# Kernel optimization log

Hardware: AMD Instinct MI355X
Metric: run time of the kernel (lower is better)

Reference implementation:

```python
import jax, jax.numpy as jnp
import numpy as np

B, S, D, H, F = 2, 2048, 1024, 16, 4096
HD = D // H
NEG_INF = jnp.float32(-1e30)


def layer_norm(x, gamma, beta, eps=1e-6):
    mu = jnp.mean(x, axis=-1, keepdims=True)
    var = jnp.mean(jnp.square(x - mu), axis=-1, keepdims=True)
    return (x - mu) * jax.lax.rsqrt(var + eps) * gamma + beta


def setup_inputs() -> dict:
    key = jax.random.key(0)
    ks = jax.random.split(key, 8)
    d = np.sqrt(float(D))
    dx_up = np.sqrt(6.0 / (D + F))
    dx_dn = np.sqrt(6.0 / (F + D))
    return {
        "x_embeds": jax.random.normal(ks[0], (B, S, D), dtype=jnp.float32),
        "tokens": jax.random.randint(ks[1], (B, S), 0, 128, dtype=jnp.int32),
        "KQV": jax.random.uniform(ks[2], (D, 3 * D), jnp.float32, -1 / d, 1 / d),
        "WO": jax.random.uniform(ks[3], (D, D), jnp.float32, -1 / d, 1 / d),
        "W_up": jax.random.uniform(ks[4], (D, F), jnp.float32, -dx_up, dx_up),
        "b_up": jnp.zeros((F,), jnp.float32),
        "W_down": jax.random.uniform(ks[5], (F, D), jnp.float32, -dx_dn, dx_dn),
        "b_down": jnp.zeros((D,), jnp.float32),
        "ln1_g": jnp.ones((D,), jnp.float32),
        "ln1_b": jnp.zeros((D,), jnp.float32),
        "ln2_g": jnp.ones((D,), jnp.float32),
        "ln2_b": jnp.zeros((D,), jnp.float32),
        "start_token_id": 1,
    }


def reference(x_embeds, tokens, KQV, WO, W_up, b_up, W_down, b_down,
              ln1_g, ln1_b, ln2_g, ln2_b, start_token_id):
    b, s = x_embeds.shape[0], x_embeds.shape[1]
    # --- attention ---
    x_kqv = jnp.einsum("bsd,de->bse", x_embeds, KQV)          # [B,S,3D]
    x_kqv = x_kqv.reshape(b, s, H, 3, HD)
    k = x_kqv[:, :, :, 0, :]   # [B,S,H,HD]
    q = x_kqv[:, :, :, 1, :]
    v = x_kqv[:, :, :, 2, :]
    inner = jnp.einsum("bqhd,bkhd->bhqk", q, k)               # [B,H,S,S]
    # causal mask
    causal = jnp.tril(jnp.ones((s, s), dtype=bool))           # [S,S]
    # block-diagonal document mask from start tokens
    seg = jnp.cumsum((tokens == start_token_id).astype(jnp.int32), axis=1)  # [B,S]
    same_seg = seg[:, :, None] == seg[:, None, :]             # [B,S,S]
    mask = causal[None, None] & same_seg[:, None]             # [B,1->H,S,S]
    inner = jnp.where(mask, inner, NEG_INF)
    dk = jnp.sqrt(jnp.float32(HD))
    WA = jax.nn.softmax(inner / dk, axis=-1)
    head_outs = jnp.einsum("bhqk,bkhd->bqhd", WA, v)          # [B,S,H,HD]
    out = head_outs.reshape(b, s, D) @ WO
    out = layer_norm(out, ln1_g, ln1_b)
    x = out + x_embeds
    # --- ffnn ---
    h = jax.nn.relu(x @ W_up + b_up)
    out = h @ W_down + b_down
    out = layer_norm(out, ln2_g, ln2_b)
    return out + x
```

## Files before the change

### kernel.cpp

```cpp
#include <hip/hip_runtime.h>

typedef unsigned short u16;
typedef unsigned int u32;
typedef __bf16 bf16_t;
typedef bf16_t bf16x8 __attribute__((ext_vector_type(8)));
typedef u16 u16x8 __attribute__((ext_vector_type(8)));
typedef float f32x4 __attribute__((ext_vector_type(4)));

__device__ __forceinline__ float bf2f(u16 u) {
    union { float f; unsigned i; } c; c.i = ((unsigned)u) << 16; return c.f;
}
__device__ __forceinline__ u16 f2bf(float f) {
    return __builtin_bit_cast(u16, (bf16_t)f);
}
__device__ __forceinline__ f32x4 mfma16(bf16x8 a, bf16x8 b, f32x4 c) {
    return __builtin_amdgcn_mfma_f32_16x16x32_bf16(a, b, c, 0, 0, 0);
}
__device__ __forceinline__ void gld16(const u16* g, u16* l) {
    __builtin_amdgcn_global_load_lds(
        (const __attribute__((address_space(1))) void*)g,
        (__attribute__((address_space(3))) void*)l, 16, 0, 0);
}

__global__ __launch_bounds__(256)
void cvt_kernel(const float* __restrict__ in, u16* __restrict__ out)
{
    const int i = (blockIdx.x * 256 + threadIdx.x) * 8;
    float4 a = *reinterpret_cast<const float4*>(in + i);
    float4 b = *reinterpret_cast<const float4*>(in + i + 4);
    u16x8 o;
    o[0] = f2bf(a.x); o[1] = f2bf(a.y); o[2] = f2bf(a.z); o[3] = f2bf(a.w);
    o[4] = f2bf(b.x); o[5] = f2bf(b.y); o[6] = f2bf(b.z); o[7] = f2bf(b.w);
    *reinterpret_cast<u16x8*>(out + i) = o;
}

__global__ __launch_bounds__(256)
void cvt_t_kernel(const float* __restrict__ in, u16* __restrict__ out,
                  int K, int N)
{
    __shared__ float tile[32][33];
    const int kb = blockIdx.x * 32, nb = blockIdx.y * 32;
    const int r = threadIdx.x >> 3, c4 = threadIdx.x & 7;
    float4 v = *reinterpret_cast<const float4*>(&in[(size_t)(kb + r) * N + nb + c4 * 4]);
    tile[r][c4 * 4 + 0] = v.x; tile[r][c4 * 4 + 1] = v.y;
    tile[r][c4 * 4 + 2] = v.z; tile[r][c4 * 4 + 3] = v.w;
    __syncthreads();
    ushort4 o;
    o.x = f2bf(tile[c4 * 4 + 0][r]);
    o.y = f2bf(tile[c4 * 4 + 1][r]);
    o.z = f2bf(tile[c4 * 4 + 2][r]);
    o.w = f2bf(tile[c4 * 4 + 3][r]);
    *reinterpret_cast<ushort4*>(&out[(size_t)(nb + r) * K + kb + c4 * 4]) = o;
}

template<int NSPLIT, bool BIAS, bool RELU, bool QSCALE>
__global__ __launch_bounds__(512, 4)
void gemm8w_kernel(const u16* __restrict__ A, const u16* __restrict__ Bt,
                   const float* __restrict__ bias, u16* __restrict__ C,
                   int M, int N, int K)
{
    __shared__ u16 As[128][64];
    __shared__ u16 Bs[128][64];
    const int tid  = threadIdx.x;
    const int lane = tid & 63;
    const int wid  = tid >> 6;
    const int wm = wid >> 2, wn = wid & 3;
    const int bm = blockIdx.x, bn = blockIdx.y;
    const int kg = lane >> 4;
    const int lc = lane & 15;
    const int pk = kg ^ ((lc + (lc >> 2)) & 3);

    f32x4 acc[4][2];
    #pragma unroll
    for (int i = 0; i < 4; ++i)
        #pragma unroll
        for (int j = 0; j < 2; ++j)
            acc[i][j] = f32x4{0.f, 0.f, 0.f, 0.f};

    const int nk = (K >> 6) / NSPLIT;
    const int kbase = (NSPLIT > 1) ? blockIdx.z * nk : 0;

    for (int kt = 0; kt < nk; ++kt) {
        const int ktg = kbase + kt;
        __syncthreads();
        #pragma unroll
        for (int p = 0; p < 2; ++p) {
            int c = p * 512 + tid;
            int row  = c >> 3;
            int half = (c >> 2) & 1;
            int ko   = (((c & 3) ^ ((row + (row >> 2)) & 3)) << 3) + half * 32;
            gld16(A + (size_t)(bm * 128 + row) * K + ktg * 64 + ko,
                  &As[0][0] + c * 8);
            gld16(Bt + (size_t)(bn * 128 + row) * K + ktg * 64 + ko,
                  &Bs[0][0] + c * 8);
        }
        __syncthreads();

        bf16x8 af[4][2], bf[2][2];
        #pragma unroll
        for (int i = 0; i < 4; ++i)
            #pragma unroll
            for (int kk = 0; kk < 2; ++kk)
                af[i][kk] = *reinterpret_cast<const bf16x8*>(
                    &As[wm * 64 + i * 16 + lc][kk * 32 + pk * 8]);
        #pragma unroll
        for (int j = 0; j < 2; ++j)
            #pragma unroll
            for (int kk = 0; kk < 2; ++kk)
                bf[j][kk] = *reinterpret_cast<const bf16x8*>(
                    &Bs[wn * 32 + j * 16 + lc][kk * 32 + pk * 8]);
        #pragma unroll
        for (int j = 0; j < 2; ++j)
            #pragma unroll
            for (int i = 0; i < 4; ++i)
                #pragma unroll
                for (int kk = 0; kk < 2; ++kk)
                    acc[i][j] = mfma16(af[i][kk], bf[j][kk], acc[i][j]);
    }

    u16* Cp = C + (size_t)((NSPLIT > 1) ? blockIdx.z : 0) * M * N;
    const bool addb = BIAS && (NSPLIT == 1 || blockIdx.z == 0);
    #pragma unroll
    for (int i = 0; i < 4; ++i) {
        #pragma unroll
        for (int j = 0; j < 2; ++j) {
            int col = bn * 128 + wn * 32 + j * 16 + lc;
            float bv = addb ? bias[col] : 0.f;
            float qs = 1.0f;
            if (QSCALE) {
                u32 cm = (u32)col % 192u;
                if (cm >= 64u && cm < 128u) qs = 0.1803368875f;
            }
            #pragma unroll
            for (int r = 0; r < 4; ++r) {
                int row = bm * 128 + wm * 64 + i * 16 + kg * 4 + r;
                float v = acc[i][j][r] + bv;
                if (RELU) v = v > 0.f ? v : 0.f;
                if (QSCALE) v *= qs;
                Cp[(size_t)row * N + col] = f2bf(v);
            }
        }
    }
}

template<int NSPLIT, bool BIAS, bool RELU>
__global__ __launch_bounds__(512, 4)
void gemm8ww_kernel(const u16* __restrict__ A, const u16* __restrict__ Bt,
                    const float* __restrict__ bias, u16* __restrict__ C,
                    int M, int N, int K)
{
    __shared__ u16 As[128][64];
    __shared__ u16 Bs[256][64];
    const int tid  = threadIdx.x;
    const int lane = tid & 63;
    const int wid  = tid >> 6;
    const int wm = wid >> 2, wn = wid & 3;
    const int bm = blockIdx.x, bn = blockIdx.y;
    const int kg = lane >> 4;
    const int lc = lane & 15;
    const int pk = kg ^ ((lc + (lc >> 2)) & 3);

    f32x4 acc[4][4];
    #pragma unroll
    for (int i = 0; i < 4; ++i)
        #pragma unroll
        for (int j = 0; j < 4; ++j)
            acc[i][j] = f32x4{0.f, 0.f, 0.f, 0.f};

    const int nk = (K >> 6) / NSPLIT;
    const int kbase = (NSPLIT > 1) ? blockIdx.z * nk : 0;

    for (int kt = 0; kt < nk; ++kt) {
        const int ktg = kbase + kt;
        __syncthreads();
        #pragma unroll
        for (int p = 0; p < 2; ++p) {
            int c = p * 512 + tid;
            int row  = c >> 3;
            int half = (c >> 2) & 1;
            int ko   = (((c & 3) ^ ((row + (row >> 2)) & 3)) << 3) + half * 32;
            gld16(A + (size_t)(bm * 128 + row) * K + ktg * 64 + ko,
                  &As[0][0] + c * 8);
        }
        #pragma unroll
        for (int p = 0; p < 4; ++p) {
            int c = p * 512 + tid;
            int row  = c >> 3;
            int half = (c >> 2) & 1;
            int ko   = (((c & 3) ^ ((row + (row >> 2)) & 3)) << 3) + half * 32;
            gld16(Bt + (size_t)(bn * 256 + row) * K + ktg * 64 + ko,
                  &Bs[0][0] + c * 8);
        }
        __syncthreads();

        #pragma unroll
        for (int kk = 0; kk < 2; ++kk) {
            bf16x8 af[4], bf[4];
            #pragma unroll
            for (int i = 0; i < 4; ++i)
                af[i] = *reinterpret_cast<const bf16x8*>(
                    &As[wm * 64 + i * 16 + lc][kk * 32 + pk * 8]);
            #pragma unroll
            for (int j = 0; j < 4; ++j)
                bf[j] = *reinterpret_cast<const bf16x8*>(
                    &Bs[wn * 64 + j * 16 + lc][kk * 32 + pk * 8]);
            #pragma unroll
            for (int j = 0; j < 4; ++j)
                #pragma unroll
                for (int i = 0; i < 4; ++i)
                    acc[i][j] = mfma16(af[i], bf[j], acc[i][j]);
        }
    }

    u16* Cp = C + (size_t)((NSPLIT > 1) ? blockIdx.z : 0) * M * N;
    const bool addb = BIAS && (NSPLIT == 1 || blockIdx.z == 0);
    #pragma unroll
    for (int i = 0; i < 4; ++i) {
        #pragma unroll
        for (int j = 0; j < 4; ++j) {
            int col = bn * 256 + wn * 64 + j * 16 + lc;
            float bv = addb ? bias[col] : 0.f;
            #pragma unroll
            for (int r = 0; r < 4; ++r) {
                int row = bm * 128 + wm * 64 + i * 16 + kg * 4 + r;
                float v = acc[i][j][r] + bv;
                if (RELU) v = v > 0.f ? v : 0.f;
                Cp[(size_t)row * N + col] = f2bf(v);
            }
        }
    }
}

__global__ __launch_bounds__(256)
void qlo_kernel(const int* __restrict__ tokens, const int* __restrict__ start_id,
                int* __restrict__ qlo)
{
    constexpr int S = 2048;
    __shared__ int part[256];
    __shared__ int pref[256];
    const int b = blockIdx.x, tid = threadIdx.x;
    const int sid = start_id[0];
    const int base = b * S + tid * 8;
    int f[8]; int loc = -1;
    #pragma unroll
    for (int j = 0; j < 8; ++j) {
        f[j] = (tokens[base + j] == sid) ? 1 : 0;
        if (f[j]) loc = tid * 8 + j;
    }
    part[tid] = loc;
    __syncthreads();
    if (tid == 0) {
        int run = -1;
        for (int i = 0; i < 256; ++i) { pref[i] = run; run = max(run, part[i]); }
    }
    __syncthreads();
    int run = pref[tid];
    #pragma unroll
    for (int j = 0; j < 8; ++j) {
        if (f[j]) run = tid * 8 + j;
        qlo[base + j] = max(run, 0);
    }
}

#define MASKVAL -60000.0f
#define MINIT   -30000.0f
__global__ __launch_bounds__(256)
void attn_kernel(const u16* __restrict__ qkv, const int* __restrict__ qloA,
                 u16* __restrict__ attn_out)
{
    constexpr int S = 2048, DQ = 3072;
    __shared__ u16 Ks[64][72];
    __shared__ u16 Vt[64][72];
    __shared__ u16 Pt[4][16][72];
    __shared__ int wm4[4];

    const int tid = threadIdx.x;
    const int lane = tid & 63, w = tid >> 6;
    const int kg = lane >> 4, lc = lane & 15;
    const int qt = blockIdx.x, h = blockIdx.y, b = blockIdx.z;
    const size_t rowbase = (size_t)b * S;
    const int colK = h * 192, colQ = colK + 64, colV = colK + 128;
    const int qrow = qt * 64 + w * 16 + lc;

    bf16x8 qf0, qf1;
    {
        const u16* qp = &qkv[(rowbase + qrow) * DQ + colQ];
        qf0 = *reinterpret_cast<const bf16x8*>(qp + kg * 8);
        qf1 = *reinterpret_cast<const bf16x8*>(qp + 32 + kg * 8);
    }
    const int myqlo = qloA[rowbase + qrow];

    int vmin = myqlo;
    #pragma unroll
    for (int m = 1; m < 16; m <<= 1) vmin = min(vmin, __shfl_xor(vmin, m));
    if (lane == 0) wm4[w] = vmin;
    __syncthreads();
    const int kb0 = min(min(wm4[0], wm4[1]), min(wm4[2], wm4[3])) >> 6;

    float m_ = MINIT, l_ = 0.f;
    f32x4 o[4];
    #pragma unroll
    for (int d = 0; d < 4; ++d) o[d] = f32x4{0.f, 0.f, 0.f, 0.f};

    const int kr = tid >> 3, kc = tid & 7;
    const int rpv = tid >> 3, chv = tid & 7;
    uint4 gk0, gk1, gv0, gv1;

    auto issue = [&](int kb) {
        const size_t base = rowbase + (size_t)kb * 64;
        gk0 = *reinterpret_cast<const uint4*>(&qkv[(base + kr) * DQ + colK + kc * 8]);
        gk1 = *reinterpret_cast<const uint4*>(&qkv[(base + 32 + kr) * DQ + colK + kc * 8]);
        const u16* vp = &qkv[(base + rpv * 2) * DQ + colV + chv * 8];
        gv0 = *reinterpret_cast<const uint4*>(vp);
        gv1 = *reinterpret_cast<const uint4*>(vp + DQ);
    };
    auto write_lds = [&]() {
        *reinterpret_cast<uint4*>(&Ks[kr][kc * 8]) = gk0;
        *reinterpret_cast<uint4*>(&Ks[32 + kr][kc * 8]) = gk1;
        u16x8 va = __builtin_bit_cast(u16x8, gv0);
        u16x8 vb = __builtin_bit_cast(u16x8, gv1);
        const int kp = (rpv * 2) ^ (chv << 3);
        #pragma unroll
        for (int j = 0; j < 8; ++j)
            *reinterpret_cast<u32*>(&Vt[chv * 8 + j][kp]) =
                (u32)va[j] | ((u32)vb[j] << 16);
    };

    issue(kb0);
    for (int kb = kb0; kb <= qt; ++kb) {
        write_lds();
        __syncthreads();
        if (kb < qt) issue(kb + 1);

        f32x4 sT[4];
        #pragma unroll
        for (int ks = 0; ks < 4; ++ks) {
            bf16x8 kf0 = *reinterpret_cast<const bf16x8*>(&Ks[ks * 16 + lc][kg * 8]);
            bf16x8 kf1 = *reinterpret_cast<const bf16x8*>(&Ks[ks * 16 + lc][32 + kg * 8]);
            f32x4 s = f32x4{0.f, 0.f, 0.f, 0.f};
            s = mfma16(kf0, qf0, s);
            s = mfma16(kf1, qf1, s);
            sT[ks] = s;
        }
        const int lo = myqlo - kb * 64, hi = qrow - kb * 64;
        #pragma unroll
        for (int ks = 0; ks < 4; ++ks) {
            #pragma unroll
            for (int r = 0; r < 4; ++r) {
                int kk = ks * 16 + kg * 4 + r;
                bool ok = (kk >= lo) && (kk <= hi);
                sT[ks][r] = ok ? sT[ks][r] : MASKVAL;
            }
        }
        float tm = fmaxf(fmaxf(fmaxf(sT[0][0], sT[0][1]), fmaxf(sT[0][2], sT[0][3])),
                         fmaxf(fmaxf(sT[1][0], sT[1][1]), fmaxf(sT[1][2], sT[1][3])));
        tm = fmaxf(tm, fmaxf(fmaxf(fmaxf(sT[2][0], sT[2][1]), fmaxf(sT[2][2], sT[2][3])),
                             fmaxf(fmaxf(sT[3][0], sT[3][1]), fmaxf(sT[3][2], sT[3][3]))));
        tm = fmaxf(tm, __shfl_xor(tm, 16));
        tm = fmaxf(tm, __shfl_xor(tm, 32));
        float mn = fmaxf(m_, tm);
        float al = exp2f(m_ - mn);
        m_ = mn;
        float ps = 0.f;
        #pragma unroll
        for (int ks = 0; ks < 4; ++ks) {
            ushort4 pw;
            float p0 = exp2f(sT[ks][0] - m_); ps += p0; pw.x = f2bf(p0);
            float p1 = exp2f(sT[ks][1] - m_); ps += p1; pw.y = f2bf(p1);
            float p2 = exp2f(sT[ks][2] - m_); ps += p2; pw.z = f2bf(p2);
            float p3 = exp2f(sT[ks][3] - m_); ps += p3; pw.w = f2bf(p3);
            *reinterpret_cast<ushort4*>(&Pt[w][lc][ks * 16 + kg * 4]) = pw;
        }
        ps += __shfl_xor(ps, 16);
        ps += __shfl_xor(ps, 32);
        l_ = l_ * al + ps;
        float alr[4];
        #pragma unroll
        for (int r = 0; r < 4; ++r) alr[r] = __shfl(al, kg * 4 + r);
        #pragma unroll
        for (int d = 0; d < 4; ++d)
            #pragma unroll
            for (int r = 0; r < 4; ++r) o[d][r] *= alr[r];

        #pragma unroll
        for (int kf = 0; kf < 2; ++kf) {
            bf16x8 pf = *reinterpret_cast<const bf16x8*>(&Pt[w][lc][kf * 32 + kg * 8]);
            #pragma unroll
            for (int d = 0; d < 4; ++d) {
                int vrow = d * 16 + lc;
                int b3 = (kf * 4 + kg) ^ ((vrow >> 3) & 7);
                bf16x8 vf = *reinterpret_cast<const bf16x8*>(&Vt[vrow][b3 * 8]);
                o[d] = mfma16(pf, vf, o[d]);
            }
        }
        __syncthreads();
    }

    float lr[4];
    #pragma unroll
    for (int r = 0; r < 4; ++r) lr[r] = __shfl(l_, kg * 4 + r);
    #pragma unroll
    for (int d = 0; d < 4; ++d)
        #pragma unroll
        for (int r = 0; r < 4; ++r) {
            float v = o[d][r] / fmaxf(lr[r], 1e-20f);
            int qo = qt * 64 + w * 16 + kg * 4 + r;
            attn_out[(rowbase + qo) * 1024 + h * 64 + d * 16 + lc] = f2bf(v);
        }
}

template<int NSPL, bool WRITE_BF>
__global__ __launch_bounds__(256)
void ln_kernel(const u16* __restrict__ in, const float* __restrict__ gam,
               const float* __restrict__ bet, const float* res,
               float* out_f, u16* __restrict__ out_bf)
{
    const int row = blockIdx.x;
    const int tid = threadIdx.x;
    const int lane = tid & 63, w = tid >> 6;
    __shared__ float red1[4], red2[4];

    const size_t base = (size_t)row * 1024 + tid * 4;
    float x0 = 0.f, x1 = 0.f, x2 = 0.f, x3 = 0.f;
    #pragma unroll
    for (int sp = 0; sp < NSPL; ++sp) {
        ushort4 xv = *reinterpret_cast<const ushort4*>(in + (size_t)sp * 4194304 + base);
        x0 += bf2f(xv.x); x1 += bf2f(xv.y); x2 += bf2f(xv.z); x3 += bf2f(xv.w);
    }

    float s = x0 + x1 + x2 + x3;
    #pragma unroll
    for (int m = 1; m < 64; m <<= 1) s += __shfl_xor(s, m);
    if (lane == 0) red1[w] = s;
    __syncthreads();
    float mu = (red1[0] + red1[1] + red1[2] + red1[3]) * (1.0f / 1024.0f);

    float d0 = x0 - mu, d1 = x1 - mu, d2 = x2 - mu, d3 = x3 - mu;
    float q = d0 * d0 + d1 * d1 + d2 * d2 + d3 * d3;
    #pragma unroll
    for (int m = 1; m < 64; m <<= 1) q += __shfl_xor(q, m);
    if (lane == 0) red2[w] = q;
    __syncthreads();
    float var = (red2[0] + red2[1] + red2[2] + red2[3]) * (1.0f / 1024.0f);
    float rs = rsqrtf(var + 1e-6f);

    float dd[4] = {d0, d1, d2, d3};
    #pragma unroll
    for (int e = 0; e < 4; ++e) {
        int col = tid * 4 + e;
        size_t idx = (size_t)row * 1024 + col;
        float y = dd[e] * rs * gam[col] + bet[col];
        float ov = y + res[idx];
        out_f[idx] = ov;
        if constexpr (WRITE_BF) out_bf[idx] = f2bf(ov);
    }
}

extern "C" void kernel_launch(void* const* d_in, const int* in_sizes, int n_in,
                              void* d_out, int out_size, void* d_ws, size_t ws_size,
                              hipStream_t stream)
{
    const float* x_emb = (const float*)d_in[0];
    const int* tokens  = (const int*)d_in[1];
    const float* KQV   = (const float*)d_in[2];
    const float* WO    = (const float*)d_in[3];
    const float* W_up  = (const float*)d_in[4];
    const float* b_up  = (const float*)d_in[5];
    const float* W_dn  = (const float*)d_in[6];
    const float* b_dn  = (const float*)d_in[7];
    const float* g1    = (const float*)d_in[8];
    const float* be1   = (const float*)d_in[9];
    const float* g2    = (const float*)d_in[10];
    const float* be2   = (const float*)d_in[11];
    const int* start   = (const int*)d_in[12];

    const size_t MiB = 1048576;
    char* ws = (char*)d_ws;
    u16* XB     = (u16*)(ws + 0);
    u16* qkv    = (u16*)(ws + 8 * MiB);
    u16* attn_o = (u16*)(ws + 32 * MiB);
    u16* KBt    = (u16*)(ws + 40 * MiB);
    int* qloA   = (int*)(ws + 46 * MiB);
    u16* WOBt   = (u16*)(ws + 0);
    u16* cpart  = (u16*)(ws + 8 * MiB);
    u16* x_bf   = (u16*)(ws + 0);
    u16* WUBt   = (u16*)(ws + 40 * MiB);
    u16* hbuf   = (u16*)(ws + 8 * MiB);
    u16* WDBt   = (u16*)(ws + 0);
    u16* fpart  = (u16*)(ws + 40 * MiB);
    float* x_f  = (float*)d_out;
    float* outp = (float*)d_out;

    cvt_kernel<<<2048, 256, 0, stream>>>(x_emb, XB);
    cvt_t_kernel<<<dim3(32, 96), 256, 0, stream>>>(KQV, KBt, 1024, 3072);
    qlo_kernel<<<2, 256, 0, stream>>>(tokens, start, qloA);
    gemm8w_kernel<1, false, false, true><<<dim3(32, 24), 512, 0, stream>>>(XB, KBt, nullptr, qkv, 4096, 3072, 1024);
    cvt_t_kernel<<<dim3(32, 32), 256, 0, stream>>>(WO, WOBt, 1024, 1024);
    attn_kernel<<<dim3(32, 16, 2), 256, 0, stream>>>(qkv, qloA, attn_o);
    cvt_t_kernel<<<dim3(32, 128), 256, 0, stream>>>(W_up, WUBt, 1024, 4096);
    gemm8w_kernel<2, false, false, false><<<dim3(32, 8, 2), 512, 0, stream>>>(attn_o, WOBt, nullptr, cpart, 4096, 1024, 1024);
    ln_kernel<2, true><<<4096, 256, 0, stream>>>(cpart, g1, be1, x_emb, x_f, x_bf);
    gemm8ww_kernel<1, true, true><<<dim3(32, 16), 512, 0, stream>>>(x_bf, WUBt, b_up, hbuf, 4096, 4096, 1024);
    cvt_t_kernel<<<dim3(128, 32), 256, 0, stream>>>(W_dn, WDBt, 4096, 1024);
    if (ws_size >= 72 * MiB) {
        gemm8ww_kernel<4, true, false><<<dim3(32, 4, 4), 512, 0, stream>>>(hbuf, WDBt, b_dn, fpart, 4096, 1024, 4096);
        ln_kernel<4, false><<<4096, 256, 0, stream>>>(fpart, g2, be2, x_f, outp, nullptr);
    } else if (ws_size >= 56 * MiB) {
        gemm8w_kernel<2, true, false, false><<<dim3(32, 8, 2), 512, 0, stream>>>(hbuf, WDBt, b_dn, fpart, 4096, 1024, 4096);
        ln_kernel<2, false><<<4096, 256, 0, stream>>>(fpart, g2, be2, x_f, outp, nullptr);
    } else {
        gemm8w_kernel<1, true, false, false><<<dim3(32, 8), 512, 0, stream>>>(hbuf, WDBt, b_dn, fpart, 4096, 1024, 4096);
        ln_kernel<1, false><<<4096, 256, 0, stream>>>(fpart, g2, be2, x_f, outp, nullptr);
    }
}
```

Baseline: 207.0 us.

## Process two query tiles per attention block to share K/V tile loads

The attention kernel now launches 512-thread blocks that each cover two adjacent 64-row query tiles, with the upper four waves on the second tile. The K/V tiles staged in LDS are shared by both, which halves global K/V traffic per query. The load work is also split: half the threads fetch V and half fetch K. In exchange the grid has half as many blocks, and the lower tile's waves sit idle at barriers during the final key block.

```diff
diff --git a/kernel.cpp b/kernel.cpp
--- a/kernel.cpp
+++ b/kernel.cpp
@@ -264,23 +264,25 @@
 
 #define MASKVAL -60000.0f
 #define MINIT   -30000.0f
-__global__ __launch_bounds__(256)
+__global__ __launch_bounds__(512)
 void attn_kernel(const u16* __restrict__ qkv, const int* __restrict__ qloA,
                  u16* __restrict__ attn_out)
 {
     constexpr int S = 2048, DQ = 3072;
     __shared__ u16 Ks[64][72];
     __shared__ u16 Vt[64][72];
-    __shared__ u16 Pt[4][16][72];
-    __shared__ int wm4[4];
+    __shared__ u16 Pt[8][16][72];
+    __shared__ int wm8[8];
 
     const int tid = threadIdx.x;
     const int lane = tid & 63, w = tid >> 6;
     const int kg = lane >> 4, lc = lane & 15;
-    const int qt = blockIdx.x, h = blockIdx.y, b = blockIdx.z;
+    const int bt = blockIdx.x, h = blockIdx.y, b = blockIdx.z;
+    const int qt_w = bt * 2 + (w >> 2);
+    const int qt_max = bt * 2 + 1;
     const size_t rowbase = (size_t)b * S;
     const int colK = h * 192, colQ = colK + 64, colV = colK + 128;
-    const int qrow = qt * 64 + w * 16 + lc;
+    const int qrow = qt_w * 64 + (w & 3) * 16 + lc;
 
     bf16x8 qf0, qf1;
     {
@@ -293,104 +295,117 @@
     int vmin = myqlo;
     #pragma unroll
     for (int m = 1; m < 16; m <<= 1) vmin = min(vmin, __shfl_xor(vmin, m));
-    if (lane == 0) wm4[w] = vmin;
+    if (lane == 0) wm8[w] = vmin;
     __syncthreads();
-    const int kb0 = min(min(wm4[0], wm4[1]), min(wm4[2], wm4[3])) >> 6;
+    int kb0v = wm8[0];
+    #pragma unroll
+    for (int i = 1; i < 8; ++i) kb0v = min(kb0v, wm8[i]);
+    const int kb0 = kb0v >> 6;
 
     float m_ = MINIT, l_ = 0.f;
     f32x4 o[4];
     #pragma unroll
     for (int d = 0; d < 4; ++d) o[d] = f32x4{0.f, 0.f, 0.f, 0.f};
 
-    const int kr = tid >> 3, kc = tid & 7;
-    const int rpv = tid >> 3, chv = tid & 7;
-    uint4 gk0, gk1, gv0, gv1;
+    const int rpv = (tid & 255) >> 3, chv = tid & 7;
+    const int tk = tid - 256;
+    uint4 gv0, gv1, gk0, gk1;
 
     auto issue = [&](int kb) {
         const size_t base = rowbase + (size_t)kb * 64;
-        gk0 = *reinterpret_cast<const uint4*>(&qkv[(base + kr) * DQ + colK + kc * 8]);
-        gk1 = *reinterpret_cast<const uint4*>(&qkv[(base + 32 + kr) * DQ + colK + kc * 8]);
-        const u16* vp = &qkv[(base + rpv * 2) * DQ + colV + chv * 8];
-        gv0 = *reinterpret_cast<const uint4*>(vp);
-        gv1 = *reinterpret_cast<const uint4*>(vp + DQ);
+        if (tid < 256) {
+            const u16* vp = &qkv[(base + rpv * 2) * DQ + colV + chv * 8];
+            gv0 = *reinterpret_cast<const uint4*>(vp);
+            gv1 = *reinterpret_cast<const uint4*>(vp + DQ);
+        } else {
+            const int kr = tk >> 3, kc = tk & 7;
+            gk0 = *reinterpret_cast<const uint4*>(&qkv[(base + kr) * DQ + colK + kc * 8]);
+            gk1 = *reinterpret_cast<const uint4*>(&qkv[(base + 32 + kr) * DQ + colK + kc * 8]);
+        }
     };
     auto write_lds = [&]() {
-        *reinterpret_cast<uint4*>(&Ks[kr][kc * 8]) = gk0;
-        *reinterpret_cast<uint4*>(&Ks[32 + kr][kc * 8]) = gk1;
-        u16x8 va = __builtin_bit_cast(u16x8, gv0);
-        u16x8 vb = __builtin_bit_cast(u16x8, gv1);
-        const int kp = (rpv * 2) ^ (chv << 3);
-        #pragma unroll
-        for (int j = 0; j < 8; ++j)
-            *reinterpret_cast<u32*>(&Vt[chv * 8 + j][kp]) =
-                (u32)va[j] | ((u32)vb[j] << 16);
+        if (tid < 256) {
+            u16x8 va = __builtin_bit_cast(u16x8, gv0);
+            u16x8 vb = __builtin_bit_cast(u16x8, gv1);
+            const int kp = (rpv * 2) ^ (chv << 3);
+            #pragma unroll
+            for (int j = 0; j < 8; ++j)
+                *reinterpret_cast<u32*>(&Vt[chv * 8 + j][kp]) =
+                    (u32)va[j] | ((u32)vb[j] << 16);
+        } else {
+            const int kr = tk >> 3, kc = tk & 7;
+            *reinterpret_cast<uint4*>(&Ks[kr][kc * 8]) = gk0;
+            *reinterpret_cast<uint4*>(&Ks[32 + kr][kc * 8]) = gk1;
+        }
     };
 
     issue(kb0);
-    for (int kb = kb0; kb <= qt; ++kb) {
+    for (int kb = kb0; kb <= qt_max; ++kb) {
         write_lds();
         __syncthreads();
-        if (kb < qt) issue(kb + 1);
-
-        f32x4 sT[4];
-        #pragma unroll
-        for (int ks = 0; ks < 4; ++ks) {
-            bf16x8 kf0 = *reinterpret_cast<const bf16x8*>(&Ks[ks * 16 + lc][kg * 8]);
-            bf16x8 kf1 = *reinterpret_cast<const bf16x8*>(&Ks[ks * 16 + lc][32 + kg * 8]);
-            f32x4 s = f32x4{0.f, 0.f, 0.f, 0.f};
-            s = mfma16(kf0, qf0, s);
-            s = mfma16(kf1, qf1, s);
-            sT[ks] = s;
-        }
-        const int lo = myqlo - kb * 64, hi = qrow - kb * 64;
-        #pragma unroll
-        for (int ks = 0; ks < 4; ++ks) {
-            #pragma unroll
-            for (int r = 0; r < 4; ++r) {
-                int kk = ks * 16 + kg * 4 + r;
-                bool ok = (kk >= lo) && (kk <= hi);
-                sT[ks][r] = ok ? sT[ks][r] : MASKVAL;
-            }
-        }
-        float tm = fmaxf(fmaxf(fmaxf(sT[0][0], sT[0][1]), fmaxf(sT[0][2], sT[0][3])),
-                         fmaxf(fmaxf(sT[1][0], sT[1][1]), fmaxf(sT[1][2], sT[1][3])));
-        tm = fmaxf(tm, fmaxf(fmaxf(fmaxf(sT[2][0], sT[2][1]), fmaxf(sT[2][2], sT[2][3])),
-                             fmaxf(fmaxf(sT[3][0], sT[3][1]), fmaxf(sT[3][2], sT[3][3]))));
-        tm = fmaxf(tm, __shfl_xor(tm, 16));
-        tm = fmaxf(tm, __shfl_xor(tm, 32));
-        float mn = fmaxf(m_, tm);
-        float al = exp2f(m_ - mn);
-        m_ = mn;
-        float ps = 0.f;
-        #pragma unroll
-        for (int ks = 0; ks < 4; ++ks) {
-            ushort4 pw;
-            float p0 = exp2f(sT[ks][0] - m_); ps += p0; pw.x = f2bf(p0);
-            float p1 = exp2f(sT[ks][1] - m_); ps += p1; pw.y = f2bf(p1);
-            float p2 = exp2f(sT[ks][2] - m_); ps += p2; pw.z = f2bf(p2);
-            float p3 = exp2f(sT[ks][3] - m_); ps += p3; pw.w = f2bf(p3);
-            *reinterpret_cast<ushort4*>(&Pt[w][lc][ks * 16 + kg * 4]) = pw;
-        }
-        ps += __shfl_xor(ps, 16);
-        ps += __shfl_xor(ps, 32);
-        l_ = l_ * al + ps;
-        float alr[4];
-        #pragma unroll
-        for (int r = 0; r < 4; ++r) alr[r] = __shfl(al, kg * 4 + r);
-        #pragma unroll
-        for (int d = 0; d < 4; ++d)
-            #pragma unroll
-            for (int r = 0; r < 4; ++r) o[d][r] *= alr[r];
-
-        #pragma unroll
-        for (int kf = 0; kf < 2; ++kf) {
-            bf16x8 pf = *reinterpret_cast<const bf16x8*>(&Pt[w][lc][kf * 32 + kg * 8]);
-            #pragma unroll
-            for (int d = 0; d < 4; ++d) {
-                int vrow = d * 16 + lc;
-                int b3 = (kf * 4 + kg) ^ ((vrow >> 3) & 7);
-                bf16x8 vf = *reinterpret_cast<const bf16x8*>(&Vt[vrow][b3 * 8]);
-                o[d] = mfma16(pf, vf, o[d]);
+        if (kb < qt_max) issue(kb + 1);
+
+        if (kb <= qt_w) {
+            f32x4 sT[4];
+            #pragma unroll
+            for (int ks = 0; ks < 4; ++ks) {
+                bf16x8 kf0 = *reinterpret_cast<const bf16x8*>(&Ks[ks * 16 + lc][kg * 8]);
+                bf16x8 kf1 = *reinterpret_cast<const bf16x8*>(&Ks[ks * 16 + lc][32 + kg * 8]);
+                f32x4 s = f32x4{0.f, 0.f, 0.f, 0.f};
+                s = mfma16(kf0, qf0, s);
+                s = mfma16(kf1, qf1, s);
+                sT[ks] = s;
+            }
+            const int lo = myqlo - kb * 64, hi = qrow - kb * 64;
+            #pragma unroll
+            for (int ks = 0; ks < 4; ++ks) {
+                #pragma unroll
+                for (int r = 0; r < 4; ++r) {
+                    int kk = ks * 16 + kg * 4 + r;
+                    bool ok = (kk >= lo) && (kk <= hi);
+                    sT[ks][r] = ok ? sT[ks][r] : MASKVAL;
+                }
+            }
+            float tm = fmaxf(fmaxf(fmaxf(sT[0][0], sT[0][1]), fmaxf(sT[0][2], sT[0][3])),
+                             fmaxf(fmaxf(sT[1][0], sT[1][1]), fmaxf(sT[1][2], sT[1][3])));
+            tm = fmaxf(tm, fmaxf(fmaxf(fmaxf(sT[2][0], sT[2][1]), fmaxf(sT[2][2], sT[2][3])),
+                                 fmaxf(fmaxf(sT[3][0], sT[3][1]), fmaxf(sT[3][2], sT[3][3]))));
+            tm = fmaxf(tm, __shfl_xor(tm, 16));
+            tm = fmaxf(tm, __shfl_xor(tm, 32));
+            float mn = fmaxf(m_, tm);
+            float al = exp2f(m_ - mn);
+            m_ = mn;
+            float ps = 0.f;
+            #pragma unroll
+            for (int ks = 0; ks < 4; ++ks) {
+                ushort4 pw;
+                float p0 = exp2f(sT[ks][0] - m_); ps += p0; pw.x = f2bf(p0);
+                float p1 = exp2f(sT[ks][1] - m_); ps += p1; pw.y = f2bf(p1);
+                float p2 = exp2f(sT[ks][2] - m_); ps += p2; pw.z = f2bf(p2);
+                float p3 = exp2f(sT[ks][3] - m_); ps += p3; pw.w = f2bf(p3);
+                *reinterpret_cast<ushort4*>(&Pt[w][lc][ks * 16 + kg * 4]) = pw;
+            }
+            ps += __shfl_xor(ps, 16);
+            ps += __shfl_xor(ps, 32);
+            l_ = l_ * al + ps;
+            float alr[4];
+            #pragma unroll
+            for (int r = 0; r < 4; ++r) alr[r] = __shfl(al, kg * 4 + r);
+            #pragma unroll
+            for (int d = 0; d < 4; ++d)
+                #pragma unroll
+                for (int r = 0; r < 4; ++r) o[d][r] *= alr[r];
+
+            #pragma unroll
+            for (int kf = 0; kf < 2; ++kf) {
+                bf16x8 pf = *reinterpret_cast<const bf16x8*>(&Pt[w][lc][kf * 32 + kg * 8]);
+                #pragma unroll
+                for (int d = 0; d < 4; ++d) {
+                    int vrow = d * 16 + lc;
+                    int b3 = (kf * 4 + kg) ^ ((vrow >> 3) & 7);
+                    bf16x8 vf = *reinterpret_cast<const bf16x8*>(&Vt[vrow][b3 * 8]);
+                    o[d] = mfma16(pf, vf, o[d]);
+                }
             }
         }
         __syncthreads();
@@ -404,7 +419,7 @@
         #pragma unroll
         for (int r = 0; r < 4; ++r) {
             float v = o[d][r] / fmaxf(lr[r], 1e-20f);
-            int qo = qt * 64 + w * 16 + kg * 4 + r;
+            int qo = qt_w * 64 + (w & 3) * 16 + kg * 4 + r;
             attn_out[(rowbase + qo) * 1024 + h * 64 + d * 16 + lc] = f2bf(v);
         }
 }
@@ -496,7 +511,7 @@
     qlo_kernel<<<2, 256, 0, stream>>>(tokens, start, qloA);
     gemm8w_kernel<1, false, false, true><<<dim3(32, 24), 512, 0, stream>>>(XB, KBt, nullptr, qkv, 4096, 3072, 1024);
     cvt_t_kernel<<<dim3(32, 32), 256, 0, stream>>>(WO, WOBt, 1024, 1024);
-    attn_kernel<<<dim3(32, 16, 2), 256, 0, stream>>>(qkv, qloA, attn_o);
+    attn_kernel<<<dim3(16, 16, 2), 512, 0, stream>>>(qkv, qloA, attn_o);
     cvt_t_kernel<<<dim3(32, 128), 256, 0, stream>>>(W_up, WUBt, 1024, 4096);
     gemm8w_kernel<2, false, false, false><<<dim3(32, 8, 2), 512, 0, stream>>>(attn_o, WOBt, nullptr, cpart, 4096, 1024, 1024);
     ln_kernel<2, true><<<4096, 256, 0, stream>>>(cpart, g1, be1, x_emb, x_f, x_bf);
```

Result: slower. 216.2 us (+4.5%).
